# Performance work log

Hardware: AMD Instinct MI355X
Metric: run time of the kernel (lower is better)

The kernel has to match this reference:

```python
import jax, jax.numpy as jnp
import numpy as np

N_IDS = 256  # vessel label ids; id 0 = background
VOL = (256, 256, 256)


def setup_inputs() -> dict:
    key = jax.random.key(0)
    k_lab, k_u, k_cls, k_par = jax.random.split(key, 4)
    vessel_labels = jax.random.randint(k_lab, VOL, 0, N_IDS, dtype=jnp.int32)
    # per-id class: 1 -> 'dark' (Uniform(0,0.8)), 0 -> 'bright' (Uniform(1.2,2))
    id_is_dark = jax.random.randint(k_cls, (N_IDS,), 0, 2, dtype=jnp.int32)
    u = jax.random.uniform(k_u, (N_IDS,), dtype=jnp.float32)
    id_intensity = jnp.where(id_is_dark == 1, 0.8 * u, 1.2 + 0.8 * u)
    # parenchyma: stands in for the stochastic noise/gamma/mul-field pipeline
    parenchyma = jax.random.normal(k_par, VOL, dtype=jnp.float32) * 0.2 + 1.0
    return {
        "vessel_labels": vessel_labels,
        "id_intensity": id_intensity,
        "id_is_dark": id_is_dark,
        "parenchyma": parenchyma,
    }


def reference(vessel_labels, id_intensity, id_is_dark, parenchyma):
    # Single-pass LUT gather replacing the per-id masked_fill_ loop.
    ids = jnp.arange(id_intensity.shape[0])
    # background id 0 keeps intensity 1.0 (scaling_tensor initialized to ones)
    intensity_lut = jnp.where(ids == 0, jnp.float32(1.0), id_intensity)
    scaling = intensity_lut[vessel_labels]                 # [D,H,W]
    mask = vessel_labels != 0                              # foreground vessels
    dark = (id_is_dark[vessel_labels] == 1) & mask
    bright = mask & ~dark
    # onehot channels: 0=background, 1=dark vessel, 2=bright vessel
    onehot = jnp.stack([~mask, dark, bright]).astype(parenchyma.dtype)  # [3,D,H,W]
    # parenchyma[vessel_mask>0] *= vessel_intensities[vessel_mask>0]
    out = jnp.where(mask, parenchyma * scaling, parenchyma)
    return out, onehot
```

## Files before the change

kernel.cpp:

```cpp
#include <hip/hip_runtime.h>


constexpr unsigned int VOX = 256u * 256u * 256u;
constexpr int N_IDS = 256;

typedef int   vint4  __attribute__((ext_vector_type(4)));
typedef float vflt4  __attribute__((ext_vector_type(4)));

__global__ __launch_bounds__(256)
void synth_semantic_kernel(const int* __restrict__ labels,
                           const float* __restrict__ id_intensity,
                           const int* __restrict__ id_is_dark,
                           const float* __restrict__ paren,
                           float* __restrict__ out)
{
    __shared__ unsigned int lut[N_IDS];
    const int t = threadIdx.x;
    {
        float sc = (t == 0) ? 1.0f : id_intensity[t];
        union { float f; unsigned int u; } cv; cv.f = sc;
        lut[t] = (cv.u & 0x7FFFFFFFu) | ((id_is_dark[t] == 1) ? 0x80000000u : 0u);
    }
    __syncthreads();

    const unsigned int lane = (unsigned int)t & 63u;
    const unsigned int wave = (blockIdx.x * 256u + (unsigned int)t) >> 6;
    const unsigned int base = wave * 1024u + lane * 4u;

    vint4 l[4]; vflt4 p[4];
#pragma unroll
    for (int g = 0; g < 4; ++g) {
        l[g] = __builtin_nontemporal_load((const vint4*)(labels + base + 256u * g));
        p[g] = __builtin_nontemporal_load((const vflt4*)(paren  + base + 256u * g));
    }

    vflt4 o[4], bg[4], dk[4], br[4];
#pragma unroll
    for (int g = 0; g < 4; ++g) {
        const int   labs[4] = {l[g].x, l[g].y, l[g].z, l[g].w};
        const float pv[4]   = {p[g].x, p[g].y, p[g].z, p[g].w};
        float oo[4], ob[4], od[4], orr[4];
#pragma unroll
        for (int j = 0; j < 4; ++j) {
            const int lab = labs[j];
            const unsigned int e = lut[lab];
            union { unsigned int u; float f; } sc; sc.u = e & 0x7FFFFFFFu;
            const bool isbg = (lab == 0);
            const bool isdk = (!isbg) && (e >> 31);
            const bool isbr = (!isbg) && !(e >> 31);
            oo[j]  = pv[j] * sc.f;
            ob[j]  = isbg ? 1.0f : 0.0f;
            od[j]  = isdk ? 1.0f : 0.0f;
            orr[j] = isbr ? 1.0f : 0.0f;
        }
        o[g]  = (vflt4){oo[0],  oo[1],  oo[2],  oo[3]};
        bg[g] = (vflt4){ob[0],  ob[1],  ob[2],  ob[3]};
        dk[g] = (vflt4){od[0],  od[1],  od[2],  od[3]};
        br[g] = (vflt4){orr[0], orr[1], orr[2], orr[3]};
    }

#pragma unroll
    for (int g = 0; g < 4; ++g)
        *(vflt4*)(out + base + 256u * g) = o[g];
#pragma unroll
    for (int g = 0; g < 4; ++g)
        *(vflt4*)(out + VOX + base + 256u * g) = bg[g];
#pragma unroll
    for (int g = 0; g < 4; ++g)
        *(vflt4*)(out + 2u * VOX + base + 256u * g) = dk[g];
#pragma unroll
    for (int g = 0; g < 4; ++g)
        *(vflt4*)(out + 3u * VOX + base + 256u * g) = br[g];
}

extern "C" void kernel_launch(void* const* d_in, const int* in_sizes, int n_in,
                              void* d_out, int out_size, void* d_ws, size_t ws_size,
                              hipStream_t stream) {
    const int*   labels  = (const int*)d_in[0];
    const float* id_int  = (const float*)d_in[1];
    const int*   id_dark = (const int*)d_in[2];
    const float* paren   = (const float*)d_in[3];
    float*       outp    = (float*)d_out;

    const unsigned int threads_total = VOX / 16u;
    const unsigned int blocks = threads_total / 256u;
    synth_semantic_kernel<<<dim3(blocks), dim3(256), 0, stream>>>(
        labels, id_int, id_dark, paren, outp);
}
```

Baseline: 361.9 us.

## Split output channels across separate block segments with nontemporal stores

```diff
diff --git a/kernel.cpp b/kernel.cpp
--- a/kernel.cpp
+++ b/kernel.cpp
@@ -23,54 +23,55 @@
     }
     __syncthreads();
 
-    const unsigned int lane = (unsigned int)t & 63u;
-    const unsigned int wave = (blockIdx.x * 256u + (unsigned int)t) >> 6;
-    const unsigned int base = wave * 1024u + lane * 4u;
+    const unsigned int seg   = blockIdx.x >> 12;
+    const unsigned int chunk = blockIdx.x & 4095u;
+    const unsigned int lane  = (unsigned int)t & 63u;
+    const unsigned int wave  = chunk * 4u + ((unsigned int)t >> 6);
+    const unsigned int base  = wave * 1024u + lane * 4u;
 
-    vint4 l[4]; vflt4 p[4];
-#pragma unroll
-    for (int g = 0; g < 4; ++g) {
-        l[g] = __builtin_nontemporal_load((const vint4*)(labels + base + 256u * g));
-        p[g] = __builtin_nontemporal_load((const vflt4*)(paren  + base + 256u * g));
-    }
-
-    vflt4 o[4], bg[4], dk[4], br[4];
-#pragma unroll
-    for (int g = 0; g < 4; ++g) {
-        const int   labs[4] = {l[g].x, l[g].y, l[g].z, l[g].w};
-        const float pv[4]   = {p[g].x, p[g].y, p[g].z, p[g].w};
-        float oo[4], ob[4], od[4], orr[4];
-#pragma unroll
-        for (int j = 0; j < 4; ++j) {
-            const int lab = labs[j];
-            const unsigned int e = lut[lab];
-            union { unsigned int u; float f; } sc; sc.u = e & 0x7FFFFFFFu;
-            const bool isbg = (lab == 0);
-            const bool isdk = (!isbg) && (e >> 31);
-            const bool isbr = (!isbg) && !(e >> 31);
-            oo[j]  = pv[j] * sc.f;
-            ob[j]  = isbg ? 1.0f : 0.0f;
-            od[j]  = isdk ? 1.0f : 0.0f;
-            orr[j] = isbr ? 1.0f : 0.0f;
-        }
-        o[g]  = (vflt4){oo[0],  oo[1],  oo[2],  oo[3]};
-        bg[g] = (vflt4){ob[0],  ob[1],  ob[2],  ob[3]};
-        dk[g] = (vflt4){od[0],  od[1],  od[2],  od[3]};
-        br[g] = (vflt4){orr[0], orr[1], orr[2], orr[3]};
-    }
-
+    vint4 l[4];
 #pragma unroll
     for (int g = 0; g < 4; ++g)
-        *(vflt4*)(out + base + 256u * g) = o[g];
+        l[g] = __builtin_nontemporal_load((const vint4*)(labels + base + 256u * g));
+
+    if (seg == 0) {
+        vflt4 p[4];
 #pragma unroll
-    for (int g = 0; g < 4; ++g)
-        *(vflt4*)(out + VOX + base + 256u * g) = bg[g];
+        for (int g = 0; g < 4; ++g)
+            p[g] = __builtin_nontemporal_load((const vflt4*)(paren + base + 256u * g));
 #pragma unroll
-    for (int g = 0; g < 4; ++g)
-        *(vflt4*)(out + 2u * VOX + base + 256u * g) = dk[g];
+        for (int g = 0; g < 4; ++g) {
+            const int   labs[4] = {l[g].x, l[g].y, l[g].z, l[g].w};
+            const float pv[4]   = {p[g].x, p[g].y, p[g].z, p[g].w};
+            float oo[4];
 #pragma unroll
-    for (int g = 0; g < 4; ++g)
-        *(vflt4*)(out + 3u * VOX + base + 256u * g) = br[g];
+            for (int j = 0; j < 4; ++j) {
+                union { unsigned int u; float f; } sc;
+                sc.u = lut[labs[j]] & 0x7FFFFFFFu;
+                oo[j] = pv[j] * sc.f;
+            }
+            const vflt4 v = (vflt4){oo[0], oo[1], oo[2], oo[3]};
+            __builtin_nontemporal_store(v, (vflt4*)(out + base + 256u * g));
+        }
+    } else {
+#pragma unroll
+        for (int g = 0; g < 4; ++g) {
+            const int labs[4] = {l[g].x, l[g].y, l[g].z, l[g].w};
+            float oo[4];
+#pragma unroll
+            for (int j = 0; j < 4; ++j) {
+                const int lab = labs[j];
+                const unsigned int darkbit = lut[lab] >> 31;
+                bool f;
+                if (seg == 1)      f = (lab == 0);
+                else if (seg == 2) f = (lab != 0) && darkbit;
+                else               f = (lab != 0) && !darkbit;
+                oo[j] = f ? 1.0f : 0.0f;
+            }
+            const vflt4 v = (vflt4){oo[0], oo[1], oo[2], oo[3]};
+            __builtin_nontemporal_store(v, (vflt4*)(out + seg * VOX + base + 256u * g));
+        }
+    }
 }
 
 extern "C" void kernel_launch(void* const* d_in, const int* in_sizes, int n_in,
@@ -82,8 +83,7 @@
     const float* paren   = (const float*)d_in[3];
     float*       outp    = (float*)d_out;
 
-    const unsigned int threads_total = VOX / 16u;
-    const unsigned int blocks = threads_total / 256u;
+    const unsigned int blocks = 4u * ((VOX / 16u) / 256u);
     synth_semantic_kernel<<<dim3(blocks), dim3(256), 0, stream>>>(
         labels, id_int, id_dark, paren, outp);
 }
```

Result: slower. 375.5 us (+3.7%).
